# Optimization experiments

Measured on AMD Instinct MI355X. Metric: run time of the kernel, lower is better.

The kernel has to match this reference:

```python
import jax, jax.numpy as jnp
import numpy as np

N, E, IN, H, OUT, L, G = 50000, 800000, 128, 128, 64, 3, 64
NEG_SLOPE = 0.2


def setup_inputs() -> dict:
    key = jax.random.key(0)
    ks = jax.random.split(key, 10)
    x = jax.random.normal(ks[0], (N, IN), dtype=jnp.float32)
    edge_index = jax.random.randint(ks[1], (2, E), 0, N, dtype=jnp.int64)
    batch = jnp.sort(jax.random.randint(ks[2], (N,), 0, G, dtype=jnp.int64))
    s_in = 1.0 / np.sqrt(IN)
    s_h = 1.0 / np.sqrt(H)
    return {
        "x": x,
        "edge_index": edge_index,
        "batch": batch,
        "W0": jax.random.normal(ks[3], (IN, H), dtype=jnp.float32) * s_in,
        "b0": jnp.zeros((H,), dtype=jnp.float32),
        "Wl": jax.random.normal(ks[4], (L, H, H), dtype=jnp.float32) * s_h,
        "a_src": jax.random.normal(ks[5], (L, H), dtype=jnp.float32) * s_h,
        "a_dst": jax.random.normal(ks[6], (L, H), dtype=jnp.float32) * s_h,
        "bl": jnp.zeros((L, H), dtype=jnp.float32),
        "Wf": jax.random.normal(ks[7], (H, OUT), dtype=jnp.float32) * s_h,
        "bf": jnp.zeros((OUT,), dtype=jnp.float32),
    }


def _gat_layer(h, src, dst, n_nodes, W, a_s, a_d, b):
    # GATConv, heads=1: h' = W h; e_ij = leaky_relu(a_s.h'_j + a_d.h'_i)
    hp = h @ W  # [N, H]
    alpha_s = hp @ a_s  # [N]
    alpha_d = hp @ a_d  # [N]
    e = jax.nn.leaky_relu(alpha_s[src] + alpha_d[dst], NEG_SLOPE)  # [E+N]
    # segment softmax over incoming edges of each destination node
    m = jax.ops.segment_max(e, dst, num_segments=n_nodes)
    ex = jnp.exp(e - m[dst])
    denom = jax.ops.segment_sum(ex, dst, num_segments=n_nodes)
    alpha = ex / denom[dst]  # [E+N]
    out = jax.ops.segment_sum(hp[src] * alpha[:, None], dst, num_segments=n_nodes)
    return out + b


def reference(x, edge_index, batch, W0, b0, Wl, a_src, a_dst, bl, Wf, bf):
    n_nodes = x.shape[0]
    loops = jnp.arange(n_nodes, dtype=edge_index.dtype)
    src = jnp.concatenate([edge_index[0], loops])  # add_self_loops=True
    dst = jnp.concatenate([edge_index[1], loops])
    h = x @ W0 + b0  # initial Linear
    n_layers = Wl.shape[0]
    for l in range(n_layers):
        h = _gat_layer(h, src, dst, n_nodes, Wl[l], a_src[l], a_dst[l], bl[l])
        if l < n_layers - 1:
            h = jax.nn.relu(h)  # BasicGNN: act between layers, none after last
    pooled = jax.ops.segment_sum(h, batch, num_segments=G)  # global_add_pool
    return (pooled @ Wf + bf).squeeze()
```

## Files before the change

kernel.cpp:

```cpp
#include <hip/hip_runtime.h>
#include <hip/hip_bf16.h>
#include <math.h>

#define HF 128
#define GCOUNT 64
#define OUTF 64
#define NEG 0.2f
#define CH 2048
#define BCAP 8192
#define PROWS 32

typedef unsigned short u16;
typedef unsigned int   u32;
typedef unsigned char  u8;
typedef short bf16x8 __attribute__((ext_vector_type(8)));
typedef float f32x4  __attribute__((ext_vector_type(4)));
typedef float f32x2  __attribute__((ext_vector_type(2)));

__device__ __forceinline__ u16 f2b(float f) {
    u32 u = __builtin_bit_cast(u32, f);
    u32 r = (u + 0x7FFFu + ((u >> 16) & 1u)) >> 16;
    return (u16)r;
}

__device__ __forceinline__ u8 f2q(float f) {
    return (u8)(__builtin_amdgcn_cvt_pk_fp8_f32(f, f, 0, false) & 0xFF);
}

__global__ void k_pack_init(const float* __restrict__ W0, const float* __restrict__ Wl,
                            u16* __restrict__ P, int* bucketCur, float* pooled) {
    if (blockIdx.x < 32) {
        int m = blockIdx.x >> 3;
        int i = (blockIdx.x & 7) * 256 + threadIdx.x;
        const float* W = (m == 0) ? W0 : Wl + (size_t)(m - 1) * HF * HF;
        u16* Pm = P + (size_t)m * HF * HF;
        int lane = i & 63, kc = (i >> 6) & 3, t = i >> 8;
        int quad = lane >> 4, col = 16 * t + (lane & 15);
        #pragma unroll
        for (int j = 0; j < 8; ++j) {
            int k = kc * 32 + quad * 8 + j;
            Pm[(size_t)i * 8 + j] = f2b(W[k * HF + col]);
        }
    } else if (blockIdx.x == 32) {
        bucketCur[threadIdx.x] = threadIdx.x * BCAP;
    } else {
        pooled[(blockIdx.x - 33) * 256 + threadIdx.x] = 0.f;
    }
}


__device__ __forceinline__ void dev_bpart(int bx, const int* __restrict__ esrc,
                                          const int* __restrict__ edst,
                                          int* __restrict__ bucketCur,
                                          u32* __restrict__ epart, int ne, int ntot) {
    __shared__ int cnt[256];
    __shared__ int base[256];
    int tid = threadIdx.x;
    int t0 = bx * CH, t1 = min(t0 + CH, ntot);
    cnt[tid] = 0;
    __syncthreads();
    int sreg[8], dreg[8];
    #pragma unroll
    for (int it = 0; it < 8; ++it) {
        int t = t0 + tid + it * 256;
        int s = 0, d = -1;
        if (t < t1) {
            if (t < ne) { s = esrc[t]; d = edst[t]; }
            else        { s = t - ne; d = s; }
            atomicAdd(&cnt[d >> 8], 1);
        }
        sreg[it] = s; dreg[it] = d;
    }
    __syncthreads();
    int c = cnt[tid];
    base[tid] = c ? atomicAdd(&bucketCur[tid], c) : 0;
    cnt[tid] = 0;
    __syncthreads();
    #pragma unroll
    for (int it = 0; it < 8; ++it) {
        int d = dreg[it];
        if (d >= 0) {
            int b = d >> 8;
            int pos = base[b] + atomicAdd(&cnt[b], 1);
            epart[pos] = ((u32)sreg[it] << 8) | (u32)(d & 255);
        }
    }
}

__device__ __forceinline__ void dev_bcsr(int bx, const u32* __restrict__ epart,
                                         const int* __restrict__ bucketCur,
                                         int* __restrict__ rowbeg,
                                         int* __restrict__ rowend,
                                         int* __restrict__ colidx, int n) {
    __shared__ int deg[256], offs[256], curs[256], s[256];
    int b = bx, tid = threadIdx.x;
    int e0 = b * BCAP, e1 = bucketCur[b];
    deg[tid] = 0;
    curs[tid] = 0;
    __syncthreads();
    for (int t = e0 + tid; t < e1; t += 256)
        atomicAdd(&deg[epart[t] & 255u], 1);
    __syncthreads();
    int v = deg[tid];
    s[tid] = v;
    __syncthreads();
    int acc = v;
    for (int off = 1; off < 256; off <<= 1) {
        int t = (tid >= off) ? s[tid - off] : 0;
        __syncthreads();
        acc += t;
        s[tid] = acc;
        __syncthreads();
    }
    int excl = acc - v;
    offs[tid] = excl;
    int node = (b << 8) + tid;
    if (node < n) {
        rowbeg[node] = e0 + excl;
        rowend[node] = e0 + excl + v;
    }
    __syncthreads();
    for (int t = e0 + tid; t < e1; t += 256) {
        u32 e = epart[t];
        int l = e & 255u;
        int pos = e0 + offs[l] + atomicAdd(&curs[l], 1);
        colidx[pos] = (int)(e >> 8);
    }
}

template<bool A32, bool Q8>
__device__ __forceinline__ void dev_gemm(int bx, const u16* __restrict__ Ab,
                                         const float* __restrict__ Af,
                                         const u16* __restrict__ Bp,
                                         const float* __restrict__ bias,
                                         const float* __restrict__ a_s,
                                         const float* __restrict__ a_d,
                                         float* __restrict__ as_,
                                         float* __restrict__ ad_,
                                         u16* __restrict__ C,
                                         u8* __restrict__ C8, int M) {
    int lane = threadIdx.x & 63;
    int wave = threadIdx.x >> 6;
    int quad = lane >> 4, l16 = lane & 15;
    int m0 = bx * 64 + wave * 16;
    int arow = m0 + l16;
    bool aval = arow < M;
    const bf16x8* Av = A32 ? nullptr : (const bf16x8*)(Ab + (size_t)arow * HF);
    const bf16x8* Bv = (const bf16x8*)Bp;
    f32x4 acc[8] = {};

    #pragma unroll
    for (int kc = 0; kc < 4; ++kc) {
        bf16x8 a = {};
        if (aval) {
            if constexpr (A32) {
                const float* ap = Af + (size_t)arow * HF + kc * 32 + quad * 8;
                float4 f0 = *(const float4*)ap;
                float4 f1 = *(const float4*)(ap + 4);
                a[0] = (short)f2b(f0.x); a[1] = (short)f2b(f0.y);
                a[2] = (short)f2b(f0.z); a[3] = (short)f2b(f0.w);
                a[4] = (short)f2b(f1.x); a[5] = (short)f2b(f1.y);
                a[6] = (short)f2b(f1.z); a[7] = (short)f2b(f1.w);
            } else {
                a = Av[kc * 4 + quad];
            }
        }
        #pragma unroll
        for (int t = 0; t < 8; ++t)
            acc[t] = __builtin_amdgcn_mfma_f32_16x16x32_bf16(a, Bv[t * 256 + kc * 64 + lane],
                                                             acc[t], 0, 0, 0);
    }

    int orow0 = m0 + quad * 4;
    #pragma unroll
    for (int t = 0; t < 8; ++t) {
        float b4 = bias ? bias[t * 16 + l16] : 0.f;
        #pragma unroll
        for (int r = 0; r < 4; ++r) {
            int orow = orow0 + r;
            if (orow < M) {
                float v = acc[t][r] + b4;
                if constexpr (Q8) C8[(size_t)orow * HF + t * 16 + l16] = f2q(v);
                else              C [(size_t)orow * HF + t * 16 + l16] = f2b(v);
            }
        }
    }

    if (as_) {
        float avs[8], avd[8];
        #pragma unroll
        for (int t = 0; t < 8; ++t) {
            avs[t] = a_s[t * 16 + l16];
            avd[t] = a_d[t * 16 + l16];
        }
        #pragma unroll
        for (int r = 0; r < 4; ++r) {
            float ps = 0.f, pd = 0.f;
            #pragma unroll
            for (int t = 0; t < 8; ++t) {
                ps = fmaf(acc[t][r], avs[t], ps);
                pd = fmaf(acc[t][r], avd[t], pd);
            }
            #pragma unroll
            for (int o = 1; o < 16; o <<= 1) {
                ps += __shfl_xor(ps, o);
                pd += __shfl_xor(pd, o);
            }
            int row = orow0 + r;
            if (l16 == 0 && row < M) { as_[row] = ps; ad_[row] = pd; }
        }
    }
}

__global__ __launch_bounds__(256) void k_gemm0_bpart(const float* __restrict__ x,
                                                     const u16* __restrict__ Wp,
                                                     const float* __restrict__ b0,
                                                     u16* __restrict__ hb, int M, int gemmb,
                                                     const int* __restrict__ esrc,
                                                     const int* __restrict__ edst,
                                                     int* __restrict__ bucketCur,
                                                     u32* __restrict__ epart, int ne, int ntot) {
    if ((int)blockIdx.x < gemmb)
        dev_gemm<true, false>(blockIdx.x, nullptr, x, Wp, b0,
                              nullptr, nullptr, nullptr, nullptr, hb, nullptr, M);
    else
        dev_bpart(blockIdx.x - gemmb, esrc, edst, bucketCur, epart, ne, ntot);
}

__global__ __launch_bounds__(256) void k_gemm1_bcsr(const u16* __restrict__ hb,
                                                    const u16* __restrict__ Bp,
                                                    const float* __restrict__ a_s,
                                                    const float* __restrict__ a_d,
                                                    float* __restrict__ as_,
                                                    float* __restrict__ ad_,
                                                    u8* __restrict__ hp8, int M, int gemmb,
                                                    const u32* __restrict__ epart,
                                                    const int* __restrict__ bucketCur,
                                                    int* __restrict__ rowbeg,
                                                    int* __restrict__ rowend,
                                                    int* __restrict__ colidx, int n) {
    if ((int)blockIdx.x < gemmb)
        dev_gemm<false, true>(blockIdx.x, hb, nullptr, Bp, nullptr,
                              a_s, a_d, as_, ad_, nullptr, hp8, M);
    else
        dev_bcsr(blockIdx.x - gemmb, epart, bucketCur, rowbeg, rowend, colidx, n);
}

__global__ __launch_bounds__(256) void k_gemm_layer(const u16* __restrict__ hb,
                                                    const u16* __restrict__ Bp,
                                                    const float* __restrict__ a_s,
                                                    const float* __restrict__ a_d,
                                                    float* __restrict__ as_,
                                                    float* __restrict__ ad_,
                                                    u8* __restrict__ hp8, int M) {
    dev_gemm<false, true>(blockIdx.x, hb, nullptr, Bp, nullptr,
                          a_s, a_d, as_, ad_, nullptr, hp8, M);
}

__global__ __launch_bounds__(256) void k_agg(const int* __restrict__ rowbeg,
                                             const int* __restrict__ rowend,
                                             const int* __restrict__ colidx,
                                             const u8* __restrict__ hp8,
                                             const float* __restrict__ as_,
                                             const float* __restrict__ ad_,
                                             const float* __restrict__ bl,
                                             u16* __restrict__ hout,
                                             int n, int relu) {
    int wave = (blockIdx.x * 256 + threadIdx.x) >> 6;
    int lane = threadIdx.x & 63;
    if (wave >= n) return;
    int beg = rowbeg[wave], end = rowend[wave];
    int deg = end - beg;
    float adi = ad_[wave];

    int  srcl = (lane < deg) ? colidx[beg + lane] : 0;
    float el = -1e30f;
    if (lane < deg) {
        float e = as_[srcl] + adi;
        el = e > 0.f ? e : NEG * e;
    }

    float m = el;
    for (int jj = beg + 64 + lane; jj < end; jj += 64) {
        float e = as_[colidx[jj]] + adi;
        e = e > 0.f ? e : NEG * e;
        m = fmaxf(m, e);
    }
    #pragma unroll
    for (int off = 32; off; off >>= 1) m = fmaxf(m, __shfl_xor(m, off));

    float ex = (lane < deg) ? __expf(el - m) : 0.f;
    float ssum = ex;
    for (int jj = beg + 64 + lane; jj < end; jj += 64) {
        float e = as_[colidx[jj]] + adi;
        e = e > 0.f ? e : NEG * e;
        ssum += __expf(e - m);
    }
    #pragma unroll
    for (int off = 32; off; off >>= 1) ssum += __shfl_xor(ssum, off);
    float wl = ex;

    int hl = lane & 31;
    int half = lane >> 5;
    float a0 = 0.f, a1 = 0.f, a2 = 0.f, a3 = 0.f;
    int cnt = deg < 64 ? deg : 64;
    int npair = (cnt + 1) >> 1;

    int p = 0;
    for (; p + 4 <= npair; p += 4) {
        #pragma unroll
        for (int i = 0; i < 4; ++i) {
            int e  = 2 * (p + i) + half;
            int ec = e < cnt ? e : cnt - 1;
            int   s = __shfl(srcl, ec);
            float w = (e < cnt) ? __shfl(wl, ec) : 0.f;
            u32 v = ((const u32*)(hp8 + (size_t)s * HF))[hl];
            f32x2 lo = __builtin_amdgcn_cvt_pk_f32_fp8((int)v, false);
            f32x2 hi = __builtin_amdgcn_cvt_pk_f32_fp8((int)v, true);
            a0 = fmaf(w, lo.x, a0); a1 = fmaf(w, lo.y, a1);
            a2 = fmaf(w, hi.x, a2); a3 = fmaf(w, hi.y, a3);
        }
    }
    for (; p < npair; ++p) {
        int e  = 2 * p + half;
        int ec = e < cnt ? e : cnt - 1;
        int   s = __shfl(srcl, ec);
        float w = (e < cnt) ? __shfl(wl, ec) : 0.f;
        u32 v = ((const u32*)(hp8 + (size_t)s * HF))[hl];
        f32x2 lo = __builtin_amdgcn_cvt_pk_f32_fp8((int)v, false);
        f32x2 hi = __builtin_amdgcn_cvt_pk_f32_fp8((int)v, true);
        a0 = fmaf(w, lo.x, a0); a1 = fmaf(w, lo.y, a1);
        a2 = fmaf(w, hi.x, a2); a3 = fmaf(w, hi.y, a3);
    }
    for (int jj = beg + 64; jj < end; ++jj) {
        int srcn = colidx[jj];
        float e = as_[srcn] + adi;
        e = e > 0.f ? e : NEG * e;
        float w = (half == 0) ? __expf(e - m) : 0.f;
        u32 v = ((const u32*)(hp8 + (size_t)srcn * HF))[hl];
        f32x2 lo = __builtin_amdgcn_cvt_pk_f32_fp8((int)v, false);
        f32x2 hi = __builtin_amdgcn_cvt_pk_f32_fp8((int)v, true);
        a0 = fmaf(w, lo.x, a0); a1 = fmaf(w, lo.y, a1);
        a2 = fmaf(w, hi.x, a2); a3 = fmaf(w, hi.y, a3);
    }

    a0 += __shfl_xor(a0, 32); a1 += __shfl_xor(a1, 32);
    a2 += __shfl_xor(a2, 32); a3 += __shfl_xor(a3, 32);

    if (half == 0) {
        float inv = 1.f / ssum;
        float4 bb = ((const float4*)bl)[hl];
        a0 = fmaf(a0, inv, bb.x); a1 = fmaf(a1, inv, bb.y);
        a2 = fmaf(a2, inv, bb.z); a3 = fmaf(a3, inv, bb.w);
        if (relu) {
            a0 = fmaxf(a0, 0.f); a1 = fmaxf(a1, 0.f);
            a2 = fmaxf(a2, 0.f); a3 = fmaxf(a3, 0.f);
        }
        uint2 o;
        o.x = ((u32)f2b(a1) << 16) | (u32)f2b(a0);
        o.y = ((u32)f2b(a3) << 16) | (u32)f2b(a2);
        ((uint2*)(hout + (size_t)wave * HF))[hl] = o;
    }
}

__global__ __launch_bounds__(128) void k_pool(const u16* __restrict__ hb,
                                              const int* __restrict__ batch,
                                              float* __restrict__ pooled, int n) {
    int r0 = blockIdx.x * PROWS;
    int r1 = min(r0 + PROWS, n);
    if (r0 >= r1) return;
    int t = threadIdx.x;
    int cur = batch[r0];
    float acc = 0.f;
    for (int i = r0; i < r1; ++i) {
        int b = batch[i];
        if (b != cur) {
            atomicAdd(&pooled[cur * HF + t], acc);
            acc = 0.f;
            cur = b;
        }
        acc += __builtin_bit_cast(float, (u32)hb[(size_t)i * HF + t] << 16);
    }
    atomicAdd(&pooled[cur * HF + t], acc);
}

__global__ void k_final(const float* __restrict__ pooled, const float* __restrict__ Wf,
                        const float* __restrict__ bf, float* __restrict__ out) {
    int g = blockIdx.x, o = threadIdx.x;
    float acc = bf[o];
    #pragma unroll 8
    for (int k = 0; k < HF; ++k) acc = fmaf(pooled[g * HF + k], Wf[k * OUTF + o], acc);
    out[g * OUTF + o] = acc;
}

extern "C" void kernel_launch(void* const* d_in, const int* in_sizes, int n_in,
                              void* d_out, int out_size, void* d_ws, size_t ws_size,
                              hipStream_t stream) {
    const float* x      = (const float*)d_in[0];
    const int*   edge   = (const int*)d_in[1];
    const int*   batch  = (const int*)d_in[2];
    const float* W0     = (const float*)d_in[3];
    const float* b0     = (const float*)d_in[4];
    const float* Wl     = (const float*)d_in[5];
    const float* a_src  = (const float*)d_in[6];
    const float* a_dst  = (const float*)d_in[7];
    const float* bl     = (const float*)d_in[8];
    const float* Wf     = (const float*)d_in[9];
    const float* bf     = (const float*)d_in[10];
    float* out = (float*)d_out;

    const int N  = in_sizes[2];
    const int E  = in_sizes[1] / 2;
    const int Et = E + N;
    const int L  = 3;
    const int NB = (N + 255) >> 8;

    char* ws = (char*)d_ws;
    size_t off = 0;
    auto alloc = [&](size_t bytes) { char* p = ws + off; off += (bytes + 255) & ~(size_t)255; return p; };
    u16*   hb      = (u16*)alloc((size_t)N * HF * 2);
    u8*    hp8     = (u8*)alloc((size_t)N * HF);
    u16*   Wp      = (u16*)alloc((size_t)4 * HF * HF * 2);
    float* as_     = (float*)alloc((size_t)N * 4);
    float* ad_     = (float*)alloc((size_t)N * 4);
    int*   rowbeg  = (int*)alloc((size_t)N * 4);
    int*   rowend  = (int*)alloc((size_t)N * 4);
    int*   colidx  = (int*)alloc((size_t)NB * BCAP * 4);
    u32*   epart   = (u32*)alloc((size_t)NB * BCAP * 4);
    int*   bucketCur = (int*)alloc(256 * 4);
    float* pooled  = (float*)alloc((size_t)GCOUNT * HF * 4);
    (void)ws_size; (void)n_in; (void)out_size;

    const int wb4   = (N + 3) / 4;
    const int gemmb = (N + 63) / 64;
    const int partb = (Et + CH - 1) / CH;

    const int* esrc = edge;
    const int* edst = edge + E;

    k_pack_init<<<65, 256, 0, stream>>>(W0, Wl, Wp, bucketCur, pooled);

    k_gemm0_bpart<<<gemmb + partb, 256, 0, stream>>>(x, Wp, b0, hb, N, gemmb,
                                                     esrc, edst, bucketCur, epart, E, Et);

    k_gemm1_bcsr<<<gemmb + NB, 256, 0, stream>>>(hb, Wp + (size_t)1 * HF * HF,
                                                 a_src, a_dst, as_, ad_, hp8, N, gemmb,
                                                 epart, bucketCur, rowbeg, rowend, colidx, N);

    for (int l = 0; l < L; ++l) {
        if (l > 0)
            k_gemm_layer<<<gemmb, 256, 0, stream>>>(hb, Wp + (size_t)(l + 1) * HF * HF,
                                                    a_src + l * HF, a_dst + l * HF,
                                                    as_, ad_, hp8, N);
        k_agg<<<wb4, 256, 0, stream>>>(rowbeg, rowend, colidx, hp8, as_, ad_, bl + l * HF, hb, N,
                                       (l < L - 1) ? 1 : 0);
    }

    k_pool<<<(N + PROWS - 1) / PROWS, 128, 0, stream>>>(hb, batch, pooled, N);
    k_final<<<GCOUNT, OUTF, 0, stream>>>(pooled, Wf, bf, out);
}
```

Measured before the change: 266.7 us.

## Fuse whole GNN pipeline into one persistent cooperative kernel with grid syncs

Replaces the sequence of about ten kernel launches with a single cooperative persistent kernel. Stages run as grid-stride loops separated by grid.sync(), and the pooling step is folded into the last aggregation through shared-memory partial sums and atomics. The aim is to remove launch overhead and inter-kernel gaps. In exchange, grid-wide barriers are added, the grid size is capped by occupancy so large stages must loop, and the larger fused kernel may use more registers and lower occupancy. If the cooperative launch fails, the old multi-kernel path still runs.

```diff
diff --git a/kernel.cpp b/kernel.cpp
--- a/kernel.cpp
+++ b/kernel.cpp
@@ -1,6 +1,9 @@
 #include <hip/hip_runtime.h>
+#include <hip/hip_cooperative_groups.h>
 #include <hip/hip_bf16.h>
 #include <math.h>
+
+namespace cg = cooperative_groups;
 
 #define HF 128
 #define GCOUNT 64
@@ -27,11 +30,14 @@
     return (u8)(__builtin_amdgcn_cvt_pk_fp8_f32(f, f, 0, false) & 0xFF);
 }
 
-__global__ void k_pack_init(const float* __restrict__ W0, const float* __restrict__ Wl,
-                            u16* __restrict__ P, int* bucketCur, float* pooled) {
-    if (blockIdx.x < 32) {
-        int m = blockIdx.x >> 3;
-        int i = (blockIdx.x & 7) * 256 + threadIdx.x;
+
+__device__ __forceinline__ void dev_pack_init(int w, const float* __restrict__ W0,
+                                              const float* __restrict__ Wl,
+                                              u16* __restrict__ P, int* bucketCur,
+                                              float* pooled) {
+    if (w < 32) {
+        int m = w >> 3;
+        int i = (w & 7) * 256 + threadIdx.x;
         const float* W = (m == 0) ? W0 : Wl + (size_t)(m - 1) * HF * HF;
         u16* Pm = P + (size_t)m * HF * HF;
         int lane = i & 63, kc = (i >> 6) & 3, t = i >> 8;
@@ -41,13 +47,12 @@
             int k = kc * 32 + quad * 8 + j;
             Pm[(size_t)i * 8 + j] = f2b(W[k * HF + col]);
         }
-    } else if (blockIdx.x == 32) {
+    } else if (w == 32) {
         bucketCur[threadIdx.x] = threadIdx.x * BCAP;
     } else {
-        pooled[(blockIdx.x - 33) * 256 + threadIdx.x] = 0.f;
-    }
-}
-
+        pooled[(w - 33) * 256 + threadIdx.x] = 0.f;
+    }
+}
 
 __device__ __forceinline__ void dev_bpart(int bx, const int* __restrict__ esrc,
                                           const int* __restrict__ edst,
@@ -212,6 +217,242 @@
     }
 }
 
+template<bool POOL>
+__device__ __forceinline__ void dev_agg_item(int it, const int* __restrict__ rowbeg,
+                                             const int* __restrict__ rowend,
+                                             const int* __restrict__ colidx,
+                                             const u8* __restrict__ hp8,
+                                             const float* __restrict__ as_,
+                                             const float* __restrict__ ad_,
+                                             const float* __restrict__ bl,
+                                             u16* __restrict__ hout,
+                                             int n, int relu,
+                                             const int* __restrict__ batch,
+                                             float* __restrict__ pooled) {
+    int wv = threadIdx.x >> 6;
+    int node = it * 4 + wv;
+    int lane = threadIdx.x & 63;
+    bool valid = node < n;
+    int beg = 0, end = 0;
+    float adi = 0.f;
+    if (valid) { beg = rowbeg[node]; end = rowend[node]; adi = ad_[node]; }
+    int deg = end - beg;
+
+    int  srcl = (lane < deg) ? colidx[beg + lane] : 0;
+    float el = -1e30f;
+    if (lane < deg) {
+        float e = as_[srcl] + adi;
+        el = e > 0.f ? e : NEG * e;
+    }
+
+    float m = el;
+    for (int jj = beg + 64 + lane; jj < end; jj += 64) {
+        float e = as_[colidx[jj]] + adi;
+        e = e > 0.f ? e : NEG * e;
+        m = fmaxf(m, e);
+    }
+    #pragma unroll
+    for (int off = 32; off; off >>= 1) m = fmaxf(m, __shfl_xor(m, off));
+
+    float ex = (lane < deg) ? __expf(el - m) : 0.f;
+    float ssum = ex;
+    for (int jj = beg + 64 + lane; jj < end; jj += 64) {
+        float e = as_[colidx[jj]] + adi;
+        e = e > 0.f ? e : NEG * e;
+        ssum += __expf(e - m);
+    }
+    #pragma unroll
+    for (int off = 32; off; off >>= 1) ssum += __shfl_xor(ssum, off);
+    float wl = ex;
+
+    int hl = lane & 31;
+    int half = lane >> 5;
+    float a0 = 0.f, a1 = 0.f, a2 = 0.f, a3 = 0.f;
+    int cnt = deg < 64 ? deg : 64;
+    int npair = (cnt + 1) >> 1;
+
+    int p = 0;
+    for (; p + 4 <= npair; p += 4) {
+        #pragma unroll
+        for (int i = 0; i < 4; ++i) {
+            int e  = 2 * (p + i) + half;
+            int ec = e < cnt ? e : cnt - 1;
+            int   s = __shfl(srcl, ec);
+            float w = (e < cnt) ? __shfl(wl, ec) : 0.f;
+            u32 v = ((const u32*)(hp8 + (size_t)s * HF))[hl];
+            f32x2 lo = __builtin_amdgcn_cvt_pk_f32_fp8((int)v, false);
+            f32x2 hi = __builtin_amdgcn_cvt_pk_f32_fp8((int)v, true);
+            a0 = fmaf(w, lo.x, a0); a1 = fmaf(w, lo.y, a1);
+            a2 = fmaf(w, hi.x, a2); a3 = fmaf(w, hi.y, a3);
+        }
+    }
+    for (; p < npair; ++p) {
+        int e  = 2 * p + half;
+        int ec = e < cnt ? e : cnt - 1;
+        int   s = __shfl(srcl, ec);
+        float w = (e < cnt) ? __shfl(wl, ec) : 0.f;
+        u32 v = ((const u32*)(hp8 + (size_t)s * HF))[hl];
+        f32x2 lo = __builtin_amdgcn_cvt_pk_f32_fp8((int)v, false);
+        f32x2 hi = __builtin_amdgcn_cvt_pk_f32_fp8((int)v, true);
+        a0 = fmaf(w, lo.x, a0); a1 = fmaf(w, lo.y, a1);
+        a2 = fmaf(w, hi.x, a2); a3 = fmaf(w, hi.y, a3);
+    }
+    for (int jj = beg + 64; jj < end; ++jj) {
+        int srcn = colidx[jj];
+        float e = as_[srcn] + adi;
+        e = e > 0.f ? e : NEG * e;
+        float w = (half == 0) ? __expf(e - m) : 0.f;
+        u32 v = ((const u32*)(hp8 + (size_t)srcn * HF))[hl];
+        f32x2 lo = __builtin_amdgcn_cvt_pk_f32_fp8((int)v, false);
+        f32x2 hi = __builtin_amdgcn_cvt_pk_f32_fp8((int)v, true);
+        a0 = fmaf(w, lo.x, a0); a1 = fmaf(w, lo.y, a1);
+        a2 = fmaf(w, hi.x, a2); a3 = fmaf(w, hi.y, a3);
+    }
+
+    a0 += __shfl_xor(a0, 32); a1 += __shfl_xor(a1, 32);
+    a2 += __shfl_xor(a2, 32); a3 += __shfl_xor(a3, 32);
+
+    if constexpr (!POOL) {
+        if (half == 0 && valid) {
+            float inv = 1.f / ssum;
+            float4 bb = ((const float4*)bl)[hl];
+            a0 = fmaf(a0, inv, bb.x); a1 = fmaf(a1, inv, bb.y);
+            a2 = fmaf(a2, inv, bb.z); a3 = fmaf(a3, inv, bb.w);
+            if (relu) {
+                a0 = fmaxf(a0, 0.f); a1 = fmaxf(a1, 0.f);
+                a2 = fmaxf(a2, 0.f); a3 = fmaxf(a3, 0.f);
+            }
+            uint2 o;
+            o.x = ((u32)f2b(a1) << 16) | (u32)f2b(a0);
+            o.y = ((u32)f2b(a3) << 16) | (u32)f2b(a2);
+            ((uint2*)(hout + (size_t)node * HF))[hl] = o;
+        }
+    } else {
+        __shared__ float ptile[4][HF];
+        if (half == 0) {
+            float o0 = 0.f, o1 = 0.f, o2 = 0.f, o3 = 0.f;
+            if (valid) {
+                float inv = 1.f / ssum;
+                float4 bb = ((const float4*)bl)[hl];
+                o0 = fmaf(a0, inv, bb.x); o1 = fmaf(a1, inv, bb.y);
+                o2 = fmaf(a2, inv, bb.z); o3 = fmaf(a3, inv, bb.w);
+            }
+            ptile[wv][hl * 4 + 0] = o0; ptile[wv][hl * 4 + 1] = o1;
+            ptile[wv][hl * 4 + 2] = o2; ptile[wv][hl * 4 + 3] = o3;
+        }
+        __syncthreads();
+        int tid = threadIdx.x;
+        if (tid < HF) {
+            float acc = 0.f;
+            int curb = -1;
+            #pragma unroll
+            for (int s2 = 0; s2 < 4; ++s2) {
+                int nd = it * 4 + s2;
+                if (nd < n) {
+                    int b = batch[nd];
+                    if (b != curb) {
+                        if (curb >= 0) atomicAdd(&pooled[curb * HF + tid], acc);
+                        curb = b;
+                        acc = 0.f;
+                    }
+                    acc += ptile[s2][tid];
+                }
+            }
+            if (curb >= 0) atomicAdd(&pooled[curb * HF + tid], acc);
+        }
+        __syncthreads();
+    }
+}
+
+struct MegaArgs {
+    const float* x; const int* esrc; const int* edst; const int* batch;
+    const float* W0; const float* b0;
+    const float* a_src; const float* a_dst; const float* bl;
+    const float* Wf; const float* bf; float* out;
+    u16* hb; u8* hp8; u16* Wp;
+    float* as_; float* ad_;
+    int* rowbeg; int* rowend; int* colidx; u32* epart; int* bucketCur;
+    float* pooled;
+    const float* Wl;
+    int N, E, Et, NB, gemmb, partb;
+};
+
+__global__ __launch_bounds__(256) void k_mega(MegaArgs A) {
+    cg::grid_group grid = cg::this_grid();
+    const int nb = gridDim.x;
+
+    for (int w = blockIdx.x; w < 65; w += nb)
+        dev_pack_init(w, A.W0, A.Wl, A.Wp, A.bucketCur, A.pooled);
+    grid.sync();
+
+    {
+        int tot = A.gemmb + A.partb;
+        for (int w = blockIdx.x; w < tot; w += nb) {
+            if (w < A.gemmb)
+                dev_gemm<true, false>(w, nullptr, A.x, A.Wp, A.b0,
+                                      nullptr, nullptr, nullptr, nullptr, A.hb, nullptr, A.N);
+            else
+                dev_bpart(w - A.gemmb, A.esrc, A.edst, A.bucketCur, A.epart, A.E, A.Et);
+        }
+    }
+    grid.sync();
+
+    {
+        int tot = A.gemmb + A.NB;
+        for (int w = blockIdx.x; w < tot; w += nb) {
+            if (w < A.gemmb)
+                dev_gemm<false, true>(w, A.hb, nullptr, A.Wp + (size_t)1 * HF * HF, nullptr,
+                                      A.a_src, A.a_dst, A.as_, A.ad_, nullptr, A.hp8, A.N);
+            else
+                dev_bcsr(w - A.gemmb, A.epart, A.bucketCur, A.rowbeg, A.rowend, A.colidx, A.N);
+        }
+    }
+    grid.sync();
+
+    const int aggItems = (A.N + 3) >> 2;
+
+    for (int it = blockIdx.x; it < aggItems; it += nb)
+        dev_agg_item<false>(it, A.rowbeg, A.rowend, A.colidx, A.hp8, A.as_, A.ad_,
+                            A.bl, A.hb, A.N, 1, nullptr, nullptr);
+    grid.sync();
+
+    for (int w = blockIdx.x; w < A.gemmb; w += nb)
+        dev_gemm<false, true>(w, A.hb, nullptr, A.Wp + (size_t)2 * HF * HF, nullptr,
+                              A.a_src + HF, A.a_dst + HF, A.as_, A.ad_, nullptr, A.hp8, A.N);
+    grid.sync();
+
+    for (int it = blockIdx.x; it < aggItems; it += nb)
+        dev_agg_item<false>(it, A.rowbeg, A.rowend, A.colidx, A.hp8, A.as_, A.ad_,
+                            A.bl + HF, A.hb, A.N, 1, nullptr, nullptr);
+    grid.sync();
+
+    for (int w = blockIdx.x; w < A.gemmb; w += nb)
+        dev_gemm<false, true>(w, A.hb, nullptr, A.Wp + (size_t)3 * HF * HF, nullptr,
+                              A.a_src + 2 * HF, A.a_dst + 2 * HF, A.as_, A.ad_, nullptr, A.hp8, A.N);
+    grid.sync();
+
+    for (int it = blockIdx.x; it < aggItems; it += nb)
+        dev_agg_item<true>(it, A.rowbeg, A.rowend, A.colidx, A.hp8, A.as_, A.ad_,
+                           A.bl + 2 * HF, nullptr, A.N, 0, A.batch, A.pooled);
+    grid.sync();
+
+    for (int g = blockIdx.x; g < GCOUNT; g += nb) {
+        int o = threadIdx.x;
+        if (o < OUTF) {
+            float acc = A.bf[o];
+            #pragma unroll 8
+            for (int k = 0; k < HF; ++k)
+                acc = fmaf(A.pooled[g * HF + k], A.Wf[k * OUTF + o], acc);
+            A.out[g * OUTF + o] = acc;
+        }
+    }
+}
+
+__global__ void k_pack_init(const float* __restrict__ W0, const float* __restrict__ Wl,
+                            u16* __restrict__ P, int* bucketCur, float* pooled) {
+    dev_pack_init(blockIdx.x, W0, Wl, P, bucketCur, pooled);
+}
+
 __global__ __launch_bounds__(256) void k_gemm0_bpart(const float* __restrict__ x,
                                                      const u16* __restrict__ Wp,
                                                      const float* __restrict__ b0,
@@ -266,101 +507,8 @@
                                              const float* __restrict__ bl,
                                              u16* __restrict__ hout,
                                              int n, int relu) {
-    int wave = (blockIdx.x * 256 + threadIdx.x) >> 6;
-    int lane = threadIdx.x & 63;
-    if (wave >= n) return;
-    int beg = rowbeg[wave], end = rowend[wave];
-    int deg = end - beg;
-    float adi = ad_[wave];
-
-    int  srcl = (lane < deg) ? colidx[beg + lane] : 0;
-    float el = -1e30f;
-    if (lane < deg) {
-        float e = as_[srcl] + adi;
-        el = e > 0.f ? e : NEG * e;
-    }
-
-    float m = el;
-    for (int jj = beg + 64 + lane; jj < end; jj += 64) {
-        float e = as_[colidx[jj]] + adi;
-        e = e > 0.f ? e : NEG * e;
-        m = fmaxf(m, e);
-    }
-    #pragma unroll
-    for (int off = 32; off; off >>= 1) m = fmaxf(m, __shfl_xor(m, off));
-
-    float ex = (lane < deg) ? __expf(el - m) : 0.f;
-    float ssum = ex;
-    for (int jj = beg + 64 + lane; jj < end; jj += 64) {
-        float e = as_[colidx[jj]] + adi;
-        e = e > 0.f ? e : NEG * e;
-        ssum += __expf(e - m);
-    }
-    #pragma unroll
-    for (int off = 32; off; off >>= 1) ssum += __shfl_xor(ssum, off);
-    float wl = ex;
-
-    int hl = lane & 31;
-    int half = lane >> 5;
-    float a0 = 0.f, a1 = 0.f, a2 = 0.f, a3 = 0.f;
-    int cnt = deg < 64 ? deg : 64;
-    int npair = (cnt + 1) >> 1;
-
-    int p = 0;
-    for (; p + 4 <= npair; p += 4) {
-        #pragma unroll
-        for (int i = 0; i < 4; ++i) {
-            int e  = 2 * (p + i) + half;
-            int ec = e < cnt ? e : cnt - 1;
-            int   s = __shfl(srcl, ec);
-            float w = (e < cnt) ? __shfl(wl, ec) : 0.f;
-            u32 v = ((const u32*)(hp8 + (size_t)s * HF))[hl];
-            f32x2 lo = __builtin_amdgcn_cvt_pk_f32_fp8((int)v, false);
-            f32x2 hi = __builtin_amdgcn_cvt_pk_f32_fp8((int)v, true);
-            a0 = fmaf(w, lo.x, a0); a1 = fmaf(w, lo.y, a1);
-            a2 = fmaf(w, hi.x, a2); a3 = fmaf(w, hi.y, a3);
-        }
-    }
-    for (; p < npair; ++p) {
-        int e  = 2 * p + half;
-        int ec = e < cnt ? e : cnt - 1;
-        int   s = __shfl(srcl, ec);
-        float w = (e < cnt) ? __shfl(wl, ec) : 0.f;
-        u32 v = ((const u32*)(hp8 + (size_t)s * HF))[hl];
-        f32x2 lo = __builtin_amdgcn_cvt_pk_f32_fp8((int)v, false);
-        f32x2 hi = __builtin_amdgcn_cvt_pk_f32_fp8((int)v, true);
-        a0 = fmaf(w, lo.x, a0); a1 = fmaf(w, lo.y, a1);
-        a2 = fmaf(w, hi.x, a2); a3 = fmaf(w, hi.y, a3);
-    }
-    for (int jj = beg + 64; jj < end; ++jj) {
-        int srcn = colidx[jj];
-        float e = as_[srcn] + adi;
-        e = e > 0.f ? e : NEG * e;
-        float w = (half == 0) ? __expf(e - m) : 0.f;
-        u32 v = ((const u32*)(hp8 + (size_t)srcn * HF))[hl];
-        f32x2 lo = __builtin_amdgcn_cvt_pk_f32_fp8((int)v, false);
-        f32x2 hi = __builtin_amdgcn_cvt_pk_f32_fp8((int)v, true);
-        a0 = fmaf(w, lo.x, a0); a1 = fmaf(w, lo.y, a1);
-        a2 = fmaf(w, hi.x, a2); a3 = fmaf(w, hi.y, a3);
-    }
-
-    a0 += __shfl_xor(a0, 32); a1 += __shfl_xor(a1, 32);
-    a2 += __shfl_xor(a2, 32); a3 += __shfl_xor(a3, 32);
-
-    if (half == 0) {
-        float inv = 1.f / ssum;
-        float4 bb = ((const float4*)bl)[hl];
-        a0 = fmaf(a0, inv, bb.x); a1 = fmaf(a1, inv, bb.y);
-        a2 = fmaf(a2, inv, bb.z); a3 = fmaf(a3, inv, bb.w);
-        if (relu) {
-            a0 = fmaxf(a0, 0.f); a1 = fmaxf(a1, 0.f);
-            a2 = fmaxf(a2, 0.f); a3 = fmaxf(a3, 0.f);
-        }
-        uint2 o;
-        o.x = ((u32)f2b(a1) << 16) | (u32)f2b(a0);
-        o.y = ((u32)f2b(a3) << 16) | (u32)f2b(a2);
-        ((uint2*)(hout + (size_t)wave * HF))[hl] = o;
-    }
+    dev_agg_item<false>(blockIdx.x, rowbeg, rowend, colidx, hp8, as_, ad_, bl,
+                        hout, n, relu, nullptr, nullptr);
 }
 
 __global__ __launch_bounds__(128) void k_pool(const u16* __restrict__ hb,
@@ -438,15 +586,41 @@
     const int* esrc = edge;
     const int* edst = edge + E;
 
+    static int g_grid = -2;
+    if (g_grid == -2) {
+        int dev = 0;
+        (void)hipGetDevice(&dev);
+        int nCU = 0;
+        (void)hipDeviceGetAttribute(&nCU, hipDeviceAttributeMultiprocessorCount, dev);
+        int perCU = 0;
+        hipError_t e = hipOccupancyMaxActiveBlocksPerMultiprocessor(&perCU, k_mega, 256, 0);
+        g_grid = (e == hipSuccess && perCU > 0 && nCU > 0) ? perCU * nCU : -1;
+    }
+
+    if (g_grid > 0) {
+        MegaArgs ha;
+        ha.x = x; ha.esrc = esrc; ha.edst = edst; ha.batch = batch;
+        ha.W0 = W0; ha.b0 = b0; ha.a_src = a_src; ha.a_dst = a_dst; ha.bl = bl;
+        ha.Wf = Wf; ha.bf = bf; ha.out = out;
+        ha.hb = hb; ha.hp8 = hp8; ha.Wp = Wp;
+        ha.as_ = as_; ha.ad_ = ad_;
+        ha.rowbeg = rowbeg; ha.rowend = rowend; ha.colidx = colidx;
+        ha.epart = epart; ha.bucketCur = bucketCur; ha.pooled = pooled;
+        ha.Wl = Wl;
+        ha.N = N; ha.E = E; ha.Et = Et; ha.NB = NB; ha.gemmb = gemmb; ha.partb = partb;
+        void* kargs[] = { (void*)&ha };
+        hipError_t err = hipLaunchCooperativeKernel((void*)k_mega, dim3(g_grid), dim3(256),
+                                                    kargs, 0, stream);
+        if (err == hipSuccess) return;
+        g_grid = -1;
+    }
+
     k_pack_init<<<65, 256, 0, stream>>>(W0, Wl, Wp, bucketCur, pooled);
-
     k_gemm0_bpart<<<gemmb + partb, 256, 0, stream>>>(x, Wp, b0, hb, N, gemmb,
                                                      esrc, edst, bucketCur, epart, E, Et);
-
     k_gemm1_bcsr<<<gemmb + NB, 256, 0, stream>>>(hb, Wp + (size_t)1 * HF * HF,
                                                  a_src, a_dst, as_, ad_, hp8, N, gemmb,
                                                  epart, bucketCur, rowbeg, rowend, colidx, N);
-
     for (int l = 0; l < L; ++l) {
         if (l > 0)
             k_gemm_layer<<<gemmb, 256, 0, stream>>>(hb, Wp + (size_t)(l + 1) * HF * HF,
@@ -455,7 +629,6 @@
         k_agg<<<wb4, 256, 0, stream>>>(rowbeg, rowend, colidx, hp8, as_, ad_, bl + l * HF, hb, N,
                                        (l < L - 1) ? 1 : 0);
     }
-
     k_pool<<<(N + PROWS - 1) / PROWS, 128, 0, stream>>>(hb, batch, pooled, N);
     k_final<<<GCOUNT, OUTF, 0, stream>>>(pooled, Wf, bf, out);
 }
```

New measurement: 895.5 us. 236% more time.
